# Optimization experiments

Measured on AMD Instinct MI355X. Metric: run time of the kernel, lower is better.

The kernel has to match this reference:

```python
import jax, jax.numpy as jnp
import numpy as np

OBS, SEQ = 8, 12          # observed steps, predicted steps (seq_len init arg)
G, P = 96, 16             # scenes x pedestrians per scene (uniform groups)
B = G * P                 # 1536
H, E, BOT, MID = 128, 64, 1024, 512


def setup_inputs() -> dict:
    key = jax.random.key(0)
    ks = jax.random.split(key, 26)
    rn = lambda k, sh, s=0.05: jax.random.normal(k, sh, jnp.float32) * s
    starts = jnp.arange(G, dtype=jnp.int64) * P
    return {
        "obs_traj": rn(ks[0], (OBS, B, 2), 1.0),
        "obs_traj_rel": rn(ks[1], (OBS, B, 2), 1.0),
        "typeID_seq": rn(ks[2], (OBS, B, 1), 1.0),
        "h0": rn(ks[3], (1, B, H), 0.1),
        "c0": rn(ks[4], (1, B, H), 0.1),
        "seq_start_end": jnp.stack([starts, starts + P], axis=1),
        # decoder spatial embedding Linear(2, E)
        "W_emb": rn(ks[5], (E, 2)), "b_emb": rn(ks[6], (E,)),
        # LSTM(E, H) weights, gate order i,f,g,o (PyTorch convention)
        "W_ih": rn(ks[7], (4 * H, E)), "b_ih": rn(ks[8], (4 * H,)),
        "W_hh": rn(ks[9], (4 * H, H)), "b_hh": rn(ks[10], (4 * H,)),
        # hidden2pos Linear(H, 2)
        "W_pos": rn(ks[11], (2, H)), "b_pos": rn(ks[12], (2,)),
        # PoolHiddenNet: spatial_embedding Linear(2, E), mlp_pre_pool [E+H, 512, BOT]
        "Wp_emb": rn(ks[13], (E, 2)), "bp_emb": rn(ks[14], (E,)),
        "Wp1": rn(ks[15], (MID, E + H)), "bp1": rn(ks[16], (MID,)),
        "Wp2": rn(ks[17], (BOT, MID)), "bp2": rn(ks[18], (BOT,)),
        # Decoder mlp [H+BOT, mlp_dim, H]
        "Wm1": rn(ks[19], (1024, H + BOT)), "bm1": rn(ks[20], (1024,)),
        "Wm2": rn(ks[21], (H, 1024)), "bm2": rn(ks[22], (H,)),
    }


def _forward(obs_traj, obs_traj_rel, h0, c0,
             W_emb, b_emb, W_ih, b_ih, W_hh, b_hh, W_pos, b_pos,
             Wp_emb, bp_emb, Wp1, bp1, Wp2, bp2, Wm1, bm1, Wm2, bm2):
    batch = obs_traj.shape[1]

    def pool(h, pos):
        # uniform groups: h_states.view(-1,H)[start:end] == reshape to (G,P,H)
        hh = h.reshape(G, P, H)
        pp = pos.reshape(G, P, 2)
        # torch semantics: row (i,j) holds pos[j]-pos[i] and hidden[j]
        rel = pp[:, None, :, :] - pp[:, :, None, :]          # (G,Pi,Pj,2)
        emb = rel @ Wp_emb.T + bp_emb                        # (G,Pi,Pj,E)
        hb = jnp.broadcast_to(hh[:, None, :, :], (G, P, P, H))
        x = jnp.concatenate([emb, hb], axis=-1)              # (G,Pi,Pj,E+H)
        x = jax.nn.relu(x @ Wp1.T + bp1)
        x = jax.nn.relu(x @ Wp2.T + bp2)                     # (G,Pi,Pj,BOT)
        return x.max(axis=2).reshape(batch, BOT)             # max over neighbors j

    def step(carry, _):
        h, c, last_pos, dec_in = carry
        gates = dec_in @ W_ih.T + b_ih + h @ W_hh.T + b_hh
        i, f, g, o = jnp.split(gates, 4, axis=-1)
        c = jax.nn.sigmoid(f) * c + jax.nn.sigmoid(i) * jnp.tanh(g)
        h = jax.nn.sigmoid(o) * jnp.tanh(c)
        rel_pos = h @ W_pos.T + b_pos                        # (B,2)
        curr_pos = rel_pos + last_pos
        pool_h = pool(h, curr_pos)
        ctx = jnp.concatenate([h, pool_h], axis=-1)          # (B,H+BOT)
        h = jax.nn.relu(jax.nn.relu(ctx @ Wm1.T + bm1) @ Wm2.T + bm2)
        dec_in = rel_pos @ W_emb.T + b_emb
        return (h, c, curr_pos, dec_in), rel_pos

    dec_in0 = obs_traj_rel[-1] @ W_emb.T + b_emb
    carry0 = (h0[0], c0[0], obs_traj[-1], dec_in0)
    (h, c, _, _), rels = jax.lax.scan(step, carry0, None, length=SEQ)
    return rels, h[None]                                     # (SEQ,B,2), (1,B,H)


def reference(obs_traj, obs_traj_rel, typeID_seq, h0, c0, seq_start_end,
              W_emb, b_emb, W_ih, b_ih, W_hh, b_hh, W_pos, b_pos,
              Wp_emb, bp_emb, Wp1, bp1, Wp2, bp2, Wm1, bm1, Wm2, bm2):
    # typeID_seq / seq_start_end unused math-wise (typeID module off; groups uniform)
    return _forward(obs_traj, obs_traj_rel, h0, c0,
                    W_emb, b_emb, W_ih, b_ih, W_hh, b_hh, W_pos, b_pos,
                    Wp_emb, bp_emb, Wp1, bp1, Wp2, bp2, Wm1, bm1, Wm2, bm2)
```

## Files before the change

kernel.cpp:

```cpp
#include <hip/hip_runtime.h>
#include <math.h>

#define OBS 8
#define SEQL 12
#define G 96
#define PP 16
#define B 1536
#define HD 128
#define ED 64
#define BOT 1024
#define MIDD 512
#define CTXD (HD + BOT)
#define MLPH 1024

typedef __attribute__((ext_vector_type(8))) short bf16x8;
typedef __attribute__((ext_vector_type(4))) float f32x4;

__device__ inline short f2bf(float x) {
    union { float f; unsigned u; } v; v.f = x;
    unsigned r = v.u + 0x7fffu + ((v.u >> 16) & 1u);
    return (short)(r >> 16);
}

__global__ void swizzleB_kernel(const float* __restrict__ src, unsigned short* __restrict__ dst,
                                int NT, int K, int total) {
    int u = blockIdx.x * 256 + threadIdx.x;
    if (u >= total) return;
    int l = u & 63; int v = u >> 6; int nt = v % NT; int kt = v / NT;
    int n = nt * 16 + (l & 15);
    int k = kt * 32 + ((l >> 4) << 3);
    const float* s = src + n * K + k;
    float4 s0 = *(const float4*)s;
    float4 s1 = *(const float4*)(s + 4);
    bf16x8 o;
    o[0] = f2bf(s0.x); o[1] = f2bf(s0.y); o[2] = f2bf(s0.z); o[3] = f2bf(s0.w);
    o[4] = f2bf(s1.x); o[5] = f2bf(s1.y); o[6] = f2bf(s1.z); o[7] = f2bf(s1.w);
    *(bf16x8*)(dst + u * 8) = o;
}

__global__ void swizzle_cat_kernel(const float* __restrict__ W_ih, const float* __restrict__ W_hh,
                                   unsigned short* __restrict__ dst) {
    int u = blockIdx.x * 256 + threadIdx.x;
    if (u >= 6 * 32 * 64) return;
    int l = u & 63; int v = u >> 6; int nt = v & 31; int kt = v >> 5;
    int n = nt * 16 + (l & 15);
    int k0 = kt * 32 + ((l >> 4) << 3);
    bf16x8 o;
#pragma unroll
    for (int e = 0; e < 8; ++e) {
        int k = k0 + e;
        float val = (k < ED) ? W_ih[n * ED + k] : W_hh[n * HD + (k - ED)];
        o[e] = f2bf(val);
    }
    *(bf16x8*)(dst + u * 8) = o;
}

__global__ void swizzle_p1_kernel(const float* __restrict__ Wp1, const float* __restrict__ M0,
                                  const float* __restrict__ M1, const float* __restrict__ CV,
                                  unsigned short* __restrict__ dst) {
    int u = blockIdx.x * 256 + threadIdx.x;
    if (u >= 5 * 32 * 64) return;
    int l = u & 63; int v = u >> 6; int nt = v & 31; int kt = v >> 5;
    int n = nt * 16 + (l & 15);
    int k0 = kt * 32 + ((l >> 4) << 3);
    bf16x8 o;
#pragma unroll
    for (int e = 0; e < 8; ++e) {
        int k = k0 + e;
        float val;
        if (k < HD)       val = Wp1[n * (ED + HD) + ED + k];
        else if (k == HD)     val = M0[n];
        else if (k == HD + 1) val = M1[n];
        else if (k == HD + 2) val = CV[n];
        else                  val = 0.f;
        o[e] = f2bf(val);
    }
    *(bf16x8*)(dst + u * 8) = o;
}

__global__ void mcvec_kernel(const float* __restrict__ Wp1, const float* __restrict__ Wp_emb,
                             const float* __restrict__ bp_emb, const float* __restrict__ bp1,
                             float* __restrict__ M0, float* __restrict__ M1, float* __restrict__ CV) {
    int r = blockIdx.x * blockDim.x + threadIdx.x;
    if (r >= MIDD) return;
    float m0 = 0.f, m1 = 0.f, cv = 0.f;
    for (int e = 0; e < ED; ++e) {
        float w = Wp1[r * (ED + HD) + e];
        m0 += w * Wp_emb[e * 2 + 0];
        m1 += w * Wp_emb[e * 2 + 1];
        cv += w * bp_emb[e];
    }
    M0[r] = m0; M1[r] = m1; CV[r] = cv + bp1[r];
}

__global__ void init_kernel(const float* __restrict__ obs_traj, const float* __restrict__ obs_traj_rel,
                            const float* __restrict__ h0, const float* __restrict__ c0,
                            const float* __restrict__ W_emb, const float* __restrict__ b_emb,
                            float* __restrict__ Hb, float* __restrict__ Cb,
                            float* __restrict__ POSb, float* __restrict__ DIN) {
    int b = blockIdx.x;
    int t = threadIdx.x;
    Hb[b * HD + t] = h0[b * HD + t];
    Cb[b * HD + t] = c0[b * HD + t];
    if (t < 2) POSb[b * 2 + t] = obs_traj[((OBS - 1) * B + b) * 2 + t];
    if (t < ED) {
        float rx = obs_traj_rel[((OBS - 1) * B + b) * 2 + 0];
        float ry = obs_traj_rel[((OBS - 1) * B + b) * 2 + 1];
        DIN[b * ED + t] = W_emb[t * 2 + 0] * rx + W_emb[t * 2 + 1] * ry + b_emb[t];
    }
}

__global__ __launch_bounds__(512) void step_kernel(
    const unsigned short* __restrict__ WcatF, const float* __restrict__ b_ih,
    const float* __restrict__ b_hh,
    const float* __restrict__ W_pos, const float* __restrict__ b_pos,
    const float* __restrict__ W_emb, const float* __restrict__ b_emb,
    const unsigned short* __restrict__ Wp1F2,
    float* __restrict__ Hb, float* __restrict__ Cb, float* __restrict__ POSb,
    float* __restrict__ DIN, unsigned short* __restrict__ Hbf,
    float* __restrict__ Ab, float* __restrict__ rel_out) {

    __shared__ unsigned short gf[6 * 64 * 8];
    __shared__ unsigned short a2f[5 * 64 * 8];
    __shared__ float hsh[16 * HD];
    __shared__ float relsh[16][4];

    int gsc = blockIdx.x;
    int t = threadIdx.x;
    int lane = t & 63, w = t >> 6;
    int colid = lane & 15, quad = lane >> 4;

    if (t < 384) {
        int kt = t >> 6;
        int j = lane & 15;
        int b = gsc * PP + j;
        int k0 = kt * 32 + ((lane >> 4) << 3);
        float4 x0, x1;
        if (k0 < ED) {
            const float4* p = (const float4*)(DIN + b * ED + k0);
            x0 = p[0]; x1 = p[1];
        } else {
            const float4* p = (const float4*)(Hb + b * HD + (k0 - ED));
            x0 = p[0]; x1 = p[1];
        }
        bf16x8 o;
        o[0] = f2bf(x0.x); o[1] = f2bf(x0.y); o[2] = f2bf(x0.z); o[3] = f2bf(x0.w);
        o[4] = f2bf(x1.x); o[5] = f2bf(x1.y); o[6] = f2bf(x1.z); o[7] = f2bf(x1.w);
        *(bf16x8*)(gf + t * 8) = o;
    }
    __syncthreads();

    f32x4 acc[4];
#pragma unroll
    for (int gi = 0; gi < 4; ++gi) acc[gi] = (f32x4)0.f;
#pragma unroll
    for (int kt = 0; kt < 6; ++kt) {
        bf16x8 af = *(const bf16x8*)(gf + (kt * 64 + lane) * 8);
#pragma unroll
        for (int gi = 0; gi < 4; ++gi) {
            bf16x8 bfr = *(const bf16x8*)(WcatF + ((kt * 32 + gi * 8 + w) * 64 + lane) * 8);
            acc[gi] = __builtin_amdgcn_mfma_f32_16x16x32_bf16(af, bfr, acc[gi], 0, 0, 0);
        }
    }
    int hcol = w * 16 + colid;
    float bias[4];
#pragma unroll
    for (int gi = 0; gi < 4; ++gi) {
        int n = (gi * 8 + w) * 16 + colid;
        bias[gi] = b_ih[n] + b_hh[n];
    }
#pragma unroll
    for (int r = 0; r < 4; ++r) {
        int row = quad * 4 + r;
        int b = gsc * PP + row;
        float gI = acc[0][r] + bias[0];
        float gF = acc[1][r] + bias[1];
        float gG = acc[2][r] + bias[2];
        float gO = acc[3][r] + bias[3];
        float c = Cb[b * HD + hcol];
        float cn = (1.f / (1.f + expf(-gF))) * c + (1.f / (1.f + expf(-gI))) * tanhf(gG);
        float hn = (1.f / (1.f + expf(-gO))) * tanhf(cn);
        Cb[b * HD + hcol] = cn;
        Hbf[b * HD + hcol] = (unsigned short)f2bf(hn);
        hsh[row * HD + hcol] = hn;
    }
    __syncthreads();

    {
        int row = t >> 5, kk = t & 31;
        float r0 = 0.f, r1 = 0.f;
#pragma unroll
        for (int q = 0; q < 4; ++q) {
            int k = kk + q * 32;
            float hv = hsh[row * HD + k];
            r0 = fmaf(hv, W_pos[k], r0);
            r1 = fmaf(hv, W_pos[HD + k], r1);
        }
#pragma unroll
        for (int m = 16; m >= 1; m >>= 1) {
            r0 += __shfl_xor(r0, m, 64);
            r1 += __shfl_xor(r1, m, 64);
        }
        if (kk == 0) {
            int b = gsc * PP + row;
            r0 += b_pos[0]; r1 += b_pos[1];
            float px = POSb[b * 2 + 0] + r0;
            float py = POSb[b * 2 + 1] + r1;
            POSb[b * 2 + 0] = px; POSb[b * 2 + 1] = py;
            rel_out[b * 2 + 0] = r0; rel_out[b * 2 + 1] = r1;
            relsh[row][0] = r0; relsh[row][1] = r1; relsh[row][2] = px; relsh[row][3] = py;
        }
    }
    __syncthreads();

#pragma unroll
    for (int rep = 0; rep < 2; ++rep) {
        int idx = rep * 512 + t;
        int row = idx >> 6, e = idx & 63;
        int b = gsc * PP + row;
        DIN[b * ED + e] = W_emb[e * 2 + 0] * relsh[row][0] +
                          W_emb[e * 2 + 1] * relsh[row][1] + b_emb[e];
    }
    if (t < 320) {
        int kt = t >> 6;
        int j = lane & 15;
        int k0 = kt * 32 + ((lane >> 4) << 3);
        bf16x8 o;
#pragma unroll
        for (int e = 0; e < 8; ++e) {
            int k = k0 + e;
            float v;
            if (k < HD)            v = hsh[j * HD + k];
            else if (k == HD)      v = relsh[j][2];
            else if (k == HD + 1)  v = relsh[j][3];
            else if (k == HD + 2)  v = 1.f;
            else                   v = 0.f;
            o[e] = f2bf(v);
        }
        *(bf16x8*)(a2f + t * 8) = o;
    }
    __syncthreads();

    f32x4 acc2[4];
#pragma unroll
    for (int q = 0; q < 4; ++q) acc2[q] = (f32x4)0.f;
#pragma unroll
    for (int kt = 0; kt < 5; ++kt) {
        bf16x8 af = *(const bf16x8*)(a2f + (kt * 64 + lane) * 8);
#pragma unroll
        for (int q = 0; q < 4; ++q) {
            bf16x8 bfr = *(const bf16x8*)(Wp1F2 + ((kt * 32 + w * 4 + q) * 64 + lane) * 8);
            acc2[q] = __builtin_amdgcn_mfma_f32_16x16x32_bf16(af, bfr, acc2[q], 0, 0, 0);
        }
    }
#pragma unroll
    for (int q = 0; q < 4; ++q)
#pragma unroll
        for (int r = 0; r < 4; ++r) {
            int b = gsc * PP + quad * 4 + r;
            Ab[b * MIDD + (w * 4 + q) * 16 + colid] = acc2[q][r];
        }
}

__global__ __launch_bounds__(256, 3) void pool_mfma4_kernel(
    const float* __restrict__ Ab, const float* __restrict__ POSb,
    const unsigned short* __restrict__ Wp2F, const float* __restrict__ bp2,
    const float* __restrict__ M0, const float* __restrict__ M1,
    unsigned short* __restrict__ POOLbf) {

    __shared__ unsigned short af_lds[8 * 4 * 64 * 8];
    __shared__ float possh[8][2];

    int bi = blockIdx.x;
    int g = bi % 96;
    int sub = bi / 96;
    int igrp = sub >> 3;
    int colq = sub & 7;
    int t = threadIdx.x, lane = t & 63, w = t >> 6;

    if (t < 16)
        possh[t >> 1][t & 1] = POSb[(g * PP + igrp * 8 + (t >> 1)) * 2 + (t & 1)];

    f32x4 acc[2][8];
#pragma unroll
    for (int p = 0; p < 2; ++p)
#pragma unroll
        for (int n = 0; n < 8; ++n) acc[p][n] = (f32x4)0.f;

    const float* Ag = Ab + g * (PP * MIDD);
    int ntb = colq * 8;

    for (int pass = 0; pass < 4; ++pass) {
        __syncthreads();
#pragma unroll
        for (int rep = 0; rep < 8; ++rep) {
            int u = rep * 256 + t;
            int ii = u >> 8;
            int ktl = (u >> 6) & 3;
            int l = u & 63;
            int j = l & 15;
            int k0 = (pass * 4 + ktl) * 32 + ((l >> 4) << 3);
            const float4* ap = (const float4*)(Ag + j * MIDD + k0);
            float4 a0 = ap[0], a1 = ap[1];
            const float4* m0p = (const float4*)(M0 + k0);
            const float4* m1p = (const float4*)(M1 + k0);
            float4 m00 = m0p[0], m01 = m0p[1];
            float4 m10 = m1p[0], m11 = m1p[1];
            float px = possh[ii][0], py = possh[ii][1];
            bf16x8 o;
            o[0] = f2bf(fmaxf(a0.x - fmaf(m00.x, px, m10.x * py), 0.f));
            o[1] = f2bf(fmaxf(a0.y - fmaf(m00.y, px, m10.y * py), 0.f));
            o[2] = f2bf(fmaxf(a0.z - fmaf(m00.z, px, m10.z * py), 0.f));
            o[3] = f2bf(fmaxf(a0.w - fmaf(m00.w, px, m10.w * py), 0.f));
            o[4] = f2bf(fmaxf(a1.x - fmaf(m01.x, px, m11.x * py), 0.f));
            o[5] = f2bf(fmaxf(a1.y - fmaf(m01.y, px, m11.y * py), 0.f));
            o[6] = f2bf(fmaxf(a1.z - fmaf(m01.z, px, m11.z * py), 0.f));
            o[7] = f2bf(fmaxf(a1.w - fmaf(m01.w, px, m11.w * py), 0.f));
            *(bf16x8*)(af_lds + u * 8) = o;
        }
        __syncthreads();
#pragma unroll
        for (int ktl = 0; ktl < 4; ++ktl) {
            int ktg = pass * 4 + ktl;
#pragma unroll
            for (int ng = 0; ng < 2; ++ng) {
                bf16x8 bfr[4];
#pragma unroll
                for (int n = 0; n < 4; ++n)
                    bfr[n] = *(const bf16x8*)(Wp2F + ((ktg * 64 + ntb + ng * 4 + n) * 64 + lane) * 8);
#pragma unroll
                for (int p = 0; p < 2; ++p) {
                    int ii = w * 2 + p;
                    bf16x8 af = *(const bf16x8*)(af_lds + ((ii * 4 + ktl) * 64 + lane) * 8);
#pragma unroll
                    for (int n = 0; n < 4; ++n)
                        acc[p][ng * 4 + n] =
                            __builtin_amdgcn_mfma_f32_16x16x32_bf16(af, bfr[n], acc[p][ng * 4 + n], 0, 0, 0);
                }
            }
        }
    }

    int quad = lane >> 4, colid = lane & 15;
#pragma unroll
    for (int p = 0; p < 2; ++p) {
        int i = g * PP + igrp * 8 + w * 2 + p;
#pragma unroll
        for (int n = 0; n < 8; ++n) {
            float m = fmaxf(fmaxf(acc[p][n][0], acc[p][n][1]),
                            fmaxf(acc[p][n][2], acc[p][n][3]));
            m = fmaxf(m, __shfl_xor(m, 16, 64));
            m = fmaxf(m, __shfl_xor(m, 32, 64));
            if (quad == 0) {
                int col = colq * 128 + n * 16 + colid;
                float v = fmaxf(m + bp2[col], 0.f);
                POOLbf[i * BOT + col] = (unsigned short)f2bf(v);
            }
        }
    }
}

__global__ __launch_bounds__(256) void mlp1_mfma_kernel(
    const unsigned short* __restrict__ Hbf, const unsigned short* __restrict__ POOLbf,
    const unsigned short* __restrict__ Wm1F, const float* __restrict__ bm1,
    unsigned short* __restrict__ Y1Mbf) {

    __shared__ unsigned short a_f[16 * 64 * 8];
    int mg = blockIdx.x;
    int ng = blockIdx.y;
    int t = threadIdx.x, lane = t & 63, w = t >> 6;
    int rh = w >> 1, nh = w & 1;

    f32x4 acc[2][2];
#pragma unroll
    for (int a = 0; a < 2; ++a)
#pragma unroll
        for (int b = 0; b < 2; ++b) acc[a][b] = (f32x4)0.f;

    for (int c = 0; c < 9; ++c) {
        __syncthreads();
#pragma unroll
        for (int u0 = 0; u0 < 1024; u0 += 256) {
            int u = u0 + t;
            int rg = u >> 8, kt = (u >> 6) & 3, l = u & 63;
            int row = mg * 64 + rg * 16 + (l & 15);
            int kl = kt * 32 + ((l >> 4) << 3);
            const unsigned short* src = (c == 0) ? (Hbf + row * HD + kl)
                                                 : (POOLbf + row * BOT + (c - 1) * 128 + kl);
            *(bf16x8*)(a_f + u * 8) = *(const bf16x8*)src;
        }
        __syncthreads();
#pragma unroll
        for (int kt = 0; kt < 4; ++kt) {
            int ktg = c * 4 + kt;
            bf16x8 bfr[2];
#pragma unroll
            for (int j = 0; j < 2; ++j) {
                int ntg = ng * 4 + nh * 2 + j;
                bfr[j] = *(const bf16x8*)(Wm1F + ((ktg * 64 + ntg) * 64 + lane) * 8);
            }
#pragma unroll
            for (int ri = 0; ri < 2; ++ri) {
                int rg = rh * 2 + ri;
                bf16x8 af = *(const bf16x8*)(a_f + ((rg * 4 + kt) * 64 + lane) * 8);
#pragma unroll
                for (int j = 0; j < 2; ++j)
                    acc[ri][j] = __builtin_amdgcn_mfma_f32_16x16x32_bf16(af, bfr[j], acc[ri][j], 0, 0, 0);
            }
        }
    }
    int quad = lane >> 4, colid = lane & 15;
#pragma unroll
    for (int ri = 0; ri < 2; ++ri)
#pragma unroll
        for (int j = 0; j < 2; ++j) {
            int col = ng * 64 + (nh * 2 + j) * 16 + colid;
            float bb = bm1[col];
#pragma unroll
            for (int r = 0; r < 4; ++r) {
                int row = mg * 64 + (rh * 2 + ri) * 16 + quad * 4 + r;
                float v = fmaxf(acc[ri][j][r] + bb, 0.f);
                Y1Mbf[row * MLPH + col] = (unsigned short)f2bf(v);
            }
        }
}

__global__ __launch_bounds__(256) void mlp2_mfma_kernel(
    const unsigned short* __restrict__ Y1Mbf, const unsigned short* __restrict__ Wm2F,
    const float* __restrict__ bm2, float* __restrict__ Hb, float* __restrict__ hout) {

    __shared__ unsigned short a_f[32 * 64 * 8];
    int rg = blockIdx.x;
    int t = threadIdx.x, lane = t & 63, w = t >> 6;

#pragma unroll
    for (int u0 = 0; u0 < 2048; u0 += 256) {
        int u = u0 + t;
        int kt = u >> 6, l = u & 63;
        int row = rg * 16 + (l & 15);
        int kl = kt * 32 + ((l >> 4) << 3);
        *(bf16x8*)(a_f + u * 8) = *(const bf16x8*)(Y1Mbf + row * MLPH + kl);
    }
    __syncthreads();

    f32x4 acc[2];
    acc[0] = (f32x4)0.f; acc[1] = (f32x4)0.f;
    for (int kt = 0; kt < 32; ++kt) {
        bf16x8 af = *(const bf16x8*)(a_f + (kt * 64 + lane) * 8);
#pragma unroll
        for (int j = 0; j < 2; ++j) {
            int ntg = w * 2 + j;
            bf16x8 bfr = *(const bf16x8*)(Wm2F + ((kt * 8 + ntg) * 64 + lane) * 8);
            acc[j] = __builtin_amdgcn_mfma_f32_16x16x32_bf16(af, bfr, acc[j], 0, 0, 0);
        }
    }
    int quad = lane >> 4, colid = lane & 15;
#pragma unroll
    for (int j = 0; j < 2; ++j) {
        int col = (w * 2 + j) * 16 + colid;
        float bb = bm2[col];
#pragma unroll
        for (int r = 0; r < 4; ++r) {
            int row = rg * 16 + quad * 4 + r;
            float v = fmaxf(acc[j][r] + bb, 0.f);
            Hb[row * HD + col] = v;
            if (hout) hout[row * HD + col] = v;
        }
    }
}

extern "C" void kernel_launch(void* const* d_in, const int* in_sizes, int n_in,
                              void* d_out, int out_size, void* d_ws, size_t ws_size,
                              hipStream_t stream) {
    const float* obs_traj     = (const float*)d_in[0];
    const float* obs_traj_rel = (const float*)d_in[1];
    const float* h0    = (const float*)d_in[3];
    const float* c0    = (const float*)d_in[4];
    const float* W_emb = (const float*)d_in[6];
    const float* b_emb = (const float*)d_in[7];
    const float* W_ih  = (const float*)d_in[8];
    const float* b_ih  = (const float*)d_in[9];
    const float* W_hh  = (const float*)d_in[10];
    const float* b_hh  = (const float*)d_in[11];
    const float* W_pos = (const float*)d_in[12];
    const float* b_pos = (const float*)d_in[13];
    const float* Wp_emb= (const float*)d_in[14];
    const float* bp_emb= (const float*)d_in[15];
    const float* Wp1   = (const float*)d_in[16];
    const float* bp1   = (const float*)d_in[17];
    const float* Wp2   = (const float*)d_in[18];
    const float* bp2   = (const float*)d_in[19];
    const float* Wm1   = (const float*)d_in[20];
    const float* bm1   = (const float*)d_in[21];
    const float* Wm2   = (const float*)d_in[22];
    const float* bm2   = (const float*)d_in[23];

    float* ws = (float*)d_ws;
    float* Hb    = ws; ws += B * HD;
    float* Cb    = ws; ws += B * HD;
    float* POSb  = ws; ws += B * 2;
    float* DIN   = ws; ws += B * ED;
    float* Ab    = ws; ws += B * MIDD;
    float* M0    = ws; ws += MIDD;
    float* M1    = ws; ws += MIDD;
    float* CV    = ws; ws += MIDD;
    unsigned short* us = (unsigned short*)ws;
    unsigned short* Hbf    = us; us += B * HD;
    unsigned short* POOLbf = us; us += B * BOT;
    unsigned short* Y1Mbf  = us; us += B * MLPH;
    unsigned short* WcatF  = us; us += 6 * 32 * 64 * 8;
    unsigned short* Wp1F2  = us; us += 5 * 32 * 64 * 8;
    unsigned short* Wp2F   = us; us += MIDD * BOT;
    unsigned short* Wm1F   = us; us += CTXD * MLPH;
    unsigned short* Wm2F   = us; us += MLPH * HD;

    float* out = (float*)d_out;
    float* rels_out = out;
    float* h_out    = out + SEQL * B * 2;

    {
        int tot = 16 * 64 * 64;
        swizzleB_kernel<<<(tot + 255) / 256, 256, 0, stream>>>(Wp2, Wp2F, 64, MIDD, tot);
        tot = 36 * 64 * 64;
        swizzleB_kernel<<<(tot + 255) / 256, 256, 0, stream>>>(Wm1, Wm1F, 64, CTXD, tot);
        tot = 32 * 8 * 64;
        swizzleB_kernel<<<(tot + 255) / 256, 256, 0, stream>>>(Wm2, Wm2F, 8, MLPH, tot);
        swizzle_cat_kernel<<<(6 * 32 * 64 + 255) / 256, 256, 0, stream>>>(W_ih, W_hh, WcatF);
    }
    mcvec_kernel<<<2, 256, 0, stream>>>(Wp1, Wp_emb, bp_emb, bp1, M0, M1, CV);
    swizzle_p1_kernel<<<(5 * 32 * 64 + 255) / 256, 256, 0, stream>>>(Wp1, M0, M1, CV, Wp1F2);
    init_kernel<<<B, 128, 0, stream>>>(obs_traj, obs_traj_rel, h0, c0, W_emb, b_emb,
                                       Hb, Cb, POSb, DIN);

    for (int s = 0; s < SEQL; ++s) {
        step_kernel<<<G, 512, 0, stream>>>(
            WcatF, b_ih, b_hh, W_pos, b_pos, W_emb, b_emb, Wp1F2,
            Hb, Cb, POSb, DIN, Hbf, Ab, rels_out + s * B * 2);
        pool_mfma4_kernel<<<G * 16, 256, 0, stream>>>(Ab, POSb, Wp2F, bp2, M0, M1, POOLbf);
        mlp1_mfma_kernel<<<dim3(24, 16), 256, 0, stream>>>(Hbf, POOLbf, Wm1F, bm1, Y1Mbf);
        mlp2_mfma_kernel<<<G, 256, 0, stream>>>(Y1Mbf, Wm2F, bm2, Hb,
                                                (s == SEQL - 1) ? h_out : (float*)nullptr);
    }
}
```

Measured before the change: 1.090 ms.

## Build pooling A-operand once per block and loop over all output columns

```diff
diff --git a/kernel.cpp b/kernel.cpp
--- a/kernel.cpp
+++ b/kernel.cpp
@@ -262,99 +262,98 @@
         }
 }
 
-__global__ __launch_bounds__(256, 3) void pool_mfma4_kernel(
+__global__ __launch_bounds__(512, 2) void pool_mfma5_kernel(
     const float* __restrict__ Ab, const float* __restrict__ POSb,
     const unsigned short* __restrict__ Wp2F, const float* __restrict__ bp2,
     const float* __restrict__ M0, const float* __restrict__ M1,
     unsigned short* __restrict__ POOLbf) {
 
-    __shared__ unsigned short af_lds[8 * 4 * 64 * 8];
+    __shared__ unsigned short af_lds[8 * 16 * 64 * 8];
     __shared__ float possh[8][2];
 
     int bi = blockIdx.x;
-    int g = bi % 96;
-    int sub = bi / 96;
-    int igrp = sub >> 3;
-    int colq = sub & 7;
+    int g = bi >> 1;
+    int igrp = bi & 1;
     int t = threadIdx.x, lane = t & 63, w = t >> 6;
 
     if (t < 16)
         possh[t >> 1][t & 1] = POSb[(g * PP + igrp * 8 + (t >> 1)) * 2 + (t & 1)];
-
-    f32x4 acc[2][8];
-#pragma unroll
-    for (int p = 0; p < 2; ++p)
-#pragma unroll
-        for (int n = 0; n < 8; ++n) acc[p][n] = (f32x4)0.f;
+    __syncthreads();
 
     const float* Ag = Ab + g * (PP * MIDD);
-    int ntb = colq * 8;
-
-    for (int pass = 0; pass < 4; ++pass) {
-        __syncthreads();
-#pragma unroll
-        for (int rep = 0; rep < 8; ++rep) {
-            int u = rep * 256 + t;
-            int ii = u >> 8;
-            int ktl = (u >> 6) & 3;
-            int l = u & 63;
-            int j = l & 15;
-            int k0 = (pass * 4 + ktl) * 32 + ((l >> 4) << 3);
-            const float4* ap = (const float4*)(Ag + j * MIDD + k0);
-            float4 a0 = ap[0], a1 = ap[1];
-            const float4* m0p = (const float4*)(M0 + k0);
-            const float4* m1p = (const float4*)(M1 + k0);
-            float4 m00 = m0p[0], m01 = m0p[1];
-            float4 m10 = m1p[0], m11 = m1p[1];
-            float px = possh[ii][0], py = possh[ii][1];
-            bf16x8 o;
-            o[0] = f2bf(fmaxf(a0.x - fmaf(m00.x, px, m10.x * py), 0.f));
-            o[1] = f2bf(fmaxf(a0.y - fmaf(m00.y, px, m10.y * py), 0.f));
-            o[2] = f2bf(fmaxf(a0.z - fmaf(m00.z, px, m10.z * py), 0.f));
-            o[3] = f2bf(fmaxf(a0.w - fmaf(m00.w, px, m10.w * py), 0.f));
-            o[4] = f2bf(fmaxf(a1.x - fmaf(m01.x, px, m11.x * py), 0.f));
-            o[5] = f2bf(fmaxf(a1.y - fmaf(m01.y, px, m11.y * py), 0.f));
-            o[6] = f2bf(fmaxf(a1.z - fmaf(m01.z, px, m11.z * py), 0.f));
-            o[7] = f2bf(fmaxf(a1.w - fmaf(m01.w, px, m11.w * py), 0.f));
-            *(bf16x8*)(af_lds + u * 8) = o;
-        }
-        __syncthreads();
-#pragma unroll
-        for (int ktl = 0; ktl < 4; ++ktl) {
-            int ktg = pass * 4 + ktl;
-#pragma unroll
-            for (int ng = 0; ng < 2; ++ng) {
+#pragma unroll
+    for (int rep = 0; rep < 16; ++rep) {
+        int u = rep * 512 + t;
+        int ii = u >> 10;
+        int kt = (u >> 6) & 15;
+        int l = u & 63;
+        int j = l & 15;
+        int k0 = kt * 32 + ((l >> 4) << 3);
+        const float4* ap = (const float4*)(Ag + j * MIDD + k0);
+        float4 a0 = ap[0], a1 = ap[1];
+        const float4* m0p = (const float4*)(M0 + k0);
+        const float4* m1p = (const float4*)(M1 + k0);
+        float4 m00 = m0p[0], m01 = m0p[1];
+        float4 m10 = m1p[0], m11 = m1p[1];
+        float px = possh[ii][0], py = possh[ii][1];
+        bf16x8 o;
+        o[0] = f2bf(fmaxf(a0.x - fmaf(m00.x, px, m10.x * py), 0.f));
+        o[1] = f2bf(fmaxf(a0.y - fmaf(m00.y, px, m10.y * py), 0.f));
+        o[2] = f2bf(fmaxf(a0.z - fmaf(m00.z, px, m10.z * py), 0.f));
+        o[3] = f2bf(fmaxf(a0.w - fmaf(m00.w, px, m10.w * py), 0.f));
+        o[4] = f2bf(fmaxf(a1.x - fmaf(m01.x, px, m11.x * py), 0.f));
+        o[5] = f2bf(fmaxf(a1.y - fmaf(m01.y, px, m11.y * py), 0.f));
+        o[6] = f2bf(fmaxf(a1.z - fmaf(m01.z, px, m11.z * py), 0.f));
+        o[7] = f2bf(fmaxf(a1.w - fmaf(m01.w, px, m11.w * py), 0.f));
+        *(bf16x8*)(af_lds + u * 8) = o;
+    }
+    __syncthreads();
+
+    int ipair = w >> 1;
+    int ntg = w & 1;
+    int ii0 = ipair * 2;
+    int quad = lane >> 4, colid = lane & 15;
+
+    for (int ncg = 0; ncg < 4; ++ncg) {
+        int ntb = ncg * 16 + ntg * 8;
+        f32x4 acc[2][8];
+#pragma unroll
+        for (int p = 0; p < 2; ++p)
+#pragma unroll
+            for (int n = 0; n < 8; ++n) acc[p][n] = (f32x4)0.f;
+
+        for (int kt = 0; kt < 16; ++kt) {
+            bf16x8 af0 = *(const bf16x8*)(af_lds + (((ii0 + 0) * 16 + kt) * 64 + lane) * 8);
+            bf16x8 af1 = *(const bf16x8*)(af_lds + (((ii0 + 1) * 16 + kt) * 64 + lane) * 8);
+#pragma unroll
+            for (int ng2 = 0; ng2 < 2; ++ng2) {
                 bf16x8 bfr[4];
 #pragma unroll
                 for (int n = 0; n < 4; ++n)
-                    bfr[n] = *(const bf16x8*)(Wp2F + ((ktg * 64 + ntb + ng * 4 + n) * 64 + lane) * 8);
-#pragma unroll
-                for (int p = 0; p < 2; ++p) {
-                    int ii = w * 2 + p;
-                    bf16x8 af = *(const bf16x8*)(af_lds + ((ii * 4 + ktl) * 64 + lane) * 8);
-#pragma unroll
-                    for (int n = 0; n < 4; ++n)
-                        acc[p][ng * 4 + n] =
-                            __builtin_amdgcn_mfma_f32_16x16x32_bf16(af, bfr[n], acc[p][ng * 4 + n], 0, 0, 0);
+                    bfr[n] = *(const bf16x8*)(Wp2F + ((kt * 64 + ntb + ng2 * 4 + n) * 64 + lane) * 8);
+#pragma unroll
+                for (int n = 0; n < 4; ++n) {
+                    acc[0][ng2 * 4 + n] =
+                        __builtin_amdgcn_mfma_f32_16x16x32_bf16(af0, bfr[n], acc[0][ng2 * 4 + n], 0, 0, 0);
+                    acc[1][ng2 * 4 + n] =
+                        __builtin_amdgcn_mfma_f32_16x16x32_bf16(af1, bfr[n], acc[1][ng2 * 4 + n], 0, 0, 0);
                 }
             }
         }
-    }
-
-    int quad = lane >> 4, colid = lane & 15;
-#pragma unroll
-    for (int p = 0; p < 2; ++p) {
-        int i = g * PP + igrp * 8 + w * 2 + p;
-#pragma unroll
-        for (int n = 0; n < 8; ++n) {
-            float m = fmaxf(fmaxf(acc[p][n][0], acc[p][n][1]),
-                            fmaxf(acc[p][n][2], acc[p][n][3]));
-            m = fmaxf(m, __shfl_xor(m, 16, 64));
-            m = fmaxf(m, __shfl_xor(m, 32, 64));
-            if (quad == 0) {
-                int col = colq * 128 + n * 16 + colid;
-                float v = fmaxf(m + bp2[col], 0.f);
-                POOLbf[i * BOT + col] = (unsigned short)f2bf(v);
+#pragma unroll
+        for (int p = 0; p < 2; ++p) {
+            int i = g * PP + igrp * 8 + ii0 + p;
+#pragma unroll
+            for (int n = 0; n < 8; ++n) {
+                float m = fmaxf(fmaxf(acc[p][n][0], acc[p][n][1]),
+                                fmaxf(acc[p][n][2], acc[p][n][3]));
+                m = fmaxf(m, __shfl_xor(m, 16, 64));
+                m = fmaxf(m, __shfl_xor(m, 32, 64));
+                if (quad == 0) {
+                    int col = (ntb + n) * 16 + colid;
+                    float v = fmaxf(m + bp2[col], 0.f);
+                    POOLbf[i * BOT + col] = (unsigned short)f2bf(v);
+                }
             }
         }
     }
@@ -536,7 +535,7 @@
         step_kernel<<<G, 512, 0, stream>>>(
             WcatF, b_ih, b_hh, W_pos, b_pos, W_emb, b_emb, Wp1F2,
             Hb, Cb, POSb, DIN, Hbf, Ab, rels_out + s * B * 2);
-        pool_mfma4_kernel<<<G * 16, 256, 0, stream>>>(Ab, POSb, Wp2F, bp2, M0, M1, POOLbf);
+        pool_mfma5_kernel<<<G * 2, 512, 0, stream>>>(Ab, POSb, Wp2F, bp2, M0, M1, POOLbf);
         mlp1_mfma_kernel<<<dim3(24, 16), 256, 0, stream>>>(Hbf, POOLbf, Wm1F, bm1, Y1Mbf);
         mlp2_mfma_kernel<<<G, 256, 0, stream>>>(Y1Mbf, Wm2F, bm2, Hb,
                                                 (s == SEQL - 1) ? h_out : (float*)nullptr);
```

Measured after the change: 1.744 ms. 59.9% more time.
